# Optimization experiments

Hardware: AMD Instinct MI355X
Metric: run time of the kernel (lower is better)

The kernel has to match this reference:

```python
import jax, jax.numpy as jnp
import numpy as np
from jax import lax

L, B, F = 1024, 2, 1024
E = 2
H = E * F          # ssm_features = 2048
N = 16             # state_dim
R = F // N         # dt_rank = 64
K = 4              # conv kernel size
DT_MIN, DT_MAX = 0.001, 0.1


def setup_inputs() -> dict:
    key = jax.random.key(0)
    ks = jax.random.split(key, 6)
    def w(k, shape, fan_in):
        return jax.random.normal(k, shape, jnp.float32) / np.float32(np.sqrt(fan_in))
    x = jax.random.normal(ks[0], (L, B, F), jnp.float32)
    W_in = w(ks[1], (F, 2 * H), F)
    W_conv = w(ks[2], (K, H // E, H), K * (H // E))  # flax Conv kernel (K, in/groups, out), groups=E
    b_conv = jnp.zeros((H,), jnp.float32)
    A_log = jnp.log(jnp.broadcast_to(jnp.arange(1, N + 1, dtype=jnp.float32), (H, N)))
    D = jnp.ones((H,), jnp.float32)
    W_ssm = w(ks[3], (H, R + 2 * N), H)
    W_dt = w(ks[4], (R, H), R)
    b_dt = jnp.zeros((H,), jnp.float32)
    W_out = w(ks[5], (H, F), H)
    return dict(x=x, W_in=W_in, W_conv=W_conv, b_conv=b_conv, A_log=A_log, D=D,
                W_ssm=W_ssm, W_dt=W_dt, b_dt=b_dt, W_out=W_out)


def _selective_scan(u, dt, A, Bm, Cm, D):
    # u, dt: (L,B,H); A: (H,N); Bm, Cm: (L,B,N); D: (H,)
    dt = jnp.clip(dt, DT_MIN, DT_MAX)
    dA = jnp.exp(jnp.einsum('lbh,hn->lbhn', dt, A))          # (L,B,H,N)
    dBu = jnp.einsum('lbh,lbn->lbhn', dt * u, Bm)            # (L,B,H,N)
    def comb(s, c):
        return (c[0] * s[0], c[0] * s[1] + c[1])
    _, xs = lax.associative_scan(comb, (dA, dBu), axis=0)
    y = jnp.einsum('lbn,lbhn->lbh', Cm, xs)
    return y + u * D


def reference(x, W_in, W_conv, b_conv, A_log, D, W_ssm, W_dt, b_dt, W_out):
    # in_proj (no bias) then split into ssm branch and gate residual
    h = x @ W_in                                             # (L,B,2H)
    xs, res = jnp.split(h, 2, axis=-1)                       # each (L,B,H)
    # causal grouped conv over time: rearrange (L,B,H)->(B,L,H), NWC layout
    xc = jnp.transpose(xs, (1, 0, 2))
    xc = lax.conv_general_dilated(
        xc, W_conv, window_strides=(1,), padding=[(K - 1, 0)],
        dimension_numbers=('NWC', 'WIO', 'NWC'), feature_group_count=E) + b_conv
    xs = jnp.transpose(xc, (1, 0, 2))                        # (L,B,H)
    u = jax.nn.silu(xs)
    # SSM
    A = -jnp.exp(A_log)                                      # (H,N)
    proj = u @ W_ssm                                         # (L,B,N+N+R)
    Bm = proj[..., :N]
    Cm = proj[..., N:2 * N]
    dt = proj[..., 2 * N:]
    delta = jax.nn.softplus(dt @ W_dt + b_dt)                # (L,B,H)
    y = _selective_scan(u, delta, A, Bm, Cm, D)
    # gate and out_proj (no bias)
    return (y * jax.nn.silu(res)) @ W_out                    # (L,B,F)
```

## Files before the change

### kernel.cpp

```cpp
#include <hip/hip_runtime.h>
#include <math.h>


typedef unsigned short u16;
typedef unsigned int u32;
typedef __attribute__((ext_vector_type(8))) short short8;
typedef __attribute__((ext_vector_type(4))) float floatx4;
typedef __attribute__((ext_vector_type(4))) u16 ushort4v;

__device__ __forceinline__ u16 f2bf(float f) {
    u32 u = __float_as_uint(f);
    return (u16)((u + 0x7fffu + ((u >> 16) & 1u)) >> 16);
}
__device__ __forceinline__ float bf2f(u16 v) {
    return __uint_as_float((u32)v << 16);
}

__device__ __forceinline__ float dpp_red16(float v) {
    v += __uint_as_float((u32)__builtin_amdgcn_update_dpp(
        0, (int)__float_as_uint(v), 0xB1, 0xF, 0xF, true));
    v += __uint_as_float((u32)__builtin_amdgcn_update_dpp(
        0, (int)__float_as_uint(v), 0x4E, 0xF, 0xF, true));
    v += __uint_as_float((u32)__builtin_amdgcn_update_dpp(
        0, (int)__float_as_uint(v), 0x141, 0xF, 0xF, true));
    v += __uint_as_float((u32)__builtin_amdgcn_update_dpp(
        0, (int)__float_as_uint(v), 0x128, 0xF, 0xF, true));
    return v;
}

__device__ __forceinline__ void gl_lds16(const u16* g, u16* l) {
    auto gp = reinterpret_cast<const __attribute__((address_space(1))) u32*>(
        reinterpret_cast<uintptr_t>(g));
    auto lp = reinterpret_cast<__attribute__((address_space(3))) u32*>(
        reinterpret_cast<uintptr_t>(l));
    __builtin_amdgcn_global_load_lds(gp, lp, 16, 0, 0);
}

__global__ __launch_bounds__(256) void trans_k(const float* __restrict__ S,
                                               u16* __restrict__ D, int R, int C)
{
    __shared__ u16 t[64][65];
    int br = blockIdx.x * 64;
    int bc = blockIdx.y * 64;
    int c = threadIdx.x & 63;
    int r0 = threadIdx.x >> 6;
#pragma unroll
    for (int i = 0; i < 16; ++i) {
        int r = r0 + i * 4;
        float v = 0.f;
        if (br + r < R && bc + c < C) v = S[(size_t)(br + r) * C + bc + c];
        t[r][c] = f2bf(v);
    }
    __syncthreads();
    int cc0 = threadIdx.x >> 4;
    int rr0 = (threadIdx.x & 15) * 4;
#pragma unroll
    for (int i = 0; i < 4; ++i) {
        int cc = i * 16 + cc0;
        if (bc + cc < C) {
            ushort4v o;
#pragma unroll
            for (int k = 0; k < 4; ++k) o[k] = t[rr0 + k][cc];
            *(ushort4v*)(D + (size_t)(bc + cc) * R + br + rr0) = o;
        }
    }
}

__global__ __launch_bounds__(256) void tbf_k(const u16* __restrict__ S,
                                             u16* __restrict__ D)
{
    __shared__ u16 t[64][68];
    int br = blockIdx.x * 64;
    int bc = blockIdx.y * 64;
    int c = threadIdx.x & 63;
    int r0 = threadIdx.x >> 6;
#pragma unroll
    for (int i = 0; i < 16; ++i) {
        int r = r0 + i * 4;
        t[r][c] = S[(size_t)(br + r) * 2048 + bc + c];
    }
    __syncthreads();
#pragma unroll
    for (int i = 0; i < 16; ++i) {
        int r = r0 + i * 4;
        D[(size_t)(bc + r) * 2048 + br + c] = t[c][r];
    }
}

__global__ __launch_bounds__(256) void cvt_k(const float* __restrict__ S, u16* __restrict__ D)
{
    int i = (blockIdx.x * 256 + threadIdx.x) * 4;
    float4 v = *(const float4*)(S + i);
    u16 o[4] = {f2bf(v.x), f2bf(v.y), f2bf(v.z), f2bf(v.w)};
    *(ulong1*)(D + i) = *(ulong1*)o;
}

__global__ __launch_bounds__(256) void cvtp_k(const float* __restrict__ proj,
                                              u16* __restrict__ pb,
                                              u16* __restrict__ bc)
{
    if (blockIdx.x < 128) {
        int g = blockIdx.x * 256 + threadIdx.x;
        int m = g >> 4, i = (g & 15) * 4;
        float4 v = *(const float4*)(proj + (size_t)m * 128 + 64 + i);
        u16 o[4] = {f2bf(v.x), f2bf(v.y), f2bf(v.z), f2bf(v.w)};
        *(ulong1*)(pb + (size_t)m * 64 + i) = *(ulong1*)o;
    } else {
        int g = (blockIdx.x - 128) * 256 + threadIdx.x;
        int m = g >> 3, i = (g & 7) * 4;
        float4 v = *(const float4*)(proj + (size_t)m * 128 + i);
        u16 o[4] = {f2bf(v.x), f2bf(v.y), f2bf(v.z), f2bf(v.w)};
        *(ulong1*)(bc + (size_t)m * 32 + i) = *(ulong1*)o;
    }
}

template<int MODE>
__global__ __launch_bounds__(256) void gls_k(
    const u16* __restrict__ A, int lda,
    const u16* __restrict__ B, int ldb,
    float* __restrict__ Cf, int ldc,
    u16* __restrict__ Cb0, u16* __restrict__ Cb1,
    const float* __restrict__ bias, int nkt)
{
    __shared__ u16 As[128 * 64];
    __shared__ u16 Bs[64 * 64];
    const int tid = threadIdx.x;
    const int bm = blockIdx.y * 128;
    const int bn = blockIdx.x * 64;
    const int gofs = (MODE == 1 && bn >= 1024) ? 1024 : 0;
    const int lane = tid & 63, wave = tid >> 6, wm = wave * 32;
    const int m16 = lane & 15, q = lane >> 4;
    floatx4 acc[2][4] = {};

    const int rsub = lane >> 3;
    const int pch  = lane & 7;

    for (int kt = 0; kt < nkt; ++kt) {
        const int k0 = kt * 64;
        int tap = 0, ck = k0;
        if (MODE == 1) { tap = k0 >> 10; ck = k0 & 1023; }
#pragma unroll
        for (int i = 0; i < 4; ++i) {
            int r = i * 32 + wave * 8 + rsub;
            int c = pch ^ (r & 7);
            const u16* g;
            if (MODE == 1) {
                int rg = bm + r + 2 * tap - 6;
                g = A + (size_t)rg * lda + gofs + ck + c * 8;
            } else {
                g = A + (size_t)(bm + r) * lda + k0 + c * 8;
            }
            gl_lds16(g, As + i * 2048 + wave * 512);
        }
#pragma unroll
        for (int i = 0; i < 2; ++i) {
            int r = i * 32 + wave * 8 + rsub;
            int c = pch ^ (r & 7);
            gl_lds16(B + (size_t)(bn + r) * ldb + k0 + c * 8,
                     Bs + i * 2048 + wave * 512);
        }
        if (MODE == 1 && bm == 0) {
            int zr = 6 - 2 * tap;
            if (zr > 0) {
                asm volatile("s_waitcnt vmcnt(0)" ::: "memory");
                if (tid < 64) {
                    int r = tid >> 3;
                    if (r < zr) *(short8*)(As + r * 64 + (tid & 7) * 8) = short8{};
                }
            }
        }
        __syncthreads();

#pragma unroll
        for (int ks = 0; ks < 2; ++ks) {
            short8 af[2], bfr[4];
#pragma unroll
            for (int ti = 0; ti < 2; ++ti) {
                int r = wm + ti * 16 + m16;
                int p = (ks * 4 + q) ^ (r & 7);
                af[ti] = *(const short8*)(As + r * 64 + p * 8);
            }
#pragma unroll
            for (int tj = 0; tj < 4; ++tj) {
                int r = tj * 16 + m16;
                int p = (ks * 4 + q) ^ (r & 7);
                bfr[tj] = *(const short8*)(Bs + r * 64 + p * 8);
            }
#pragma unroll
            for (int ti = 0; ti < 2; ++ti)
#pragma unroll
                for (int tj = 0; tj < 4; ++tj)
                    acc[ti][tj] = __builtin_amdgcn_mfma_f32_16x16x32_bf16(
                        af[ti], bfr[tj], acc[ti][tj], 0, 0, 0);
        }
        __syncthreads();
    }

    if (MODE == 2) {
#pragma unroll
        for (int tj = 0; tj < 4; ++tj) {
            int gn = bn + tj * 16 + m16;
#pragma unroll
            for (int ti = 0; ti < 2; ++ti) {
                int gm0 = bm + wm + ti * 16 + q * 4;
#pragma unroll
                for (int r = 0; r < 4; ++r)
                    Cf[(size_t)(gm0 + r) * ldc + gn] = acc[ti][tj][r];
            }
        }
        return;
    }
    if (MODE == 0 && bn >= 2048) {
#pragma unroll
        for (int tj = 0; tj < 4; ++tj) {
            int gn = bn + tj * 16 + m16;
#pragma unroll
            for (int ti = 0; ti < 2; ++ti) {
                int gm0 = bm + wm + ti * 16 + q * 4;
                ushort4v h;
#pragma unroll
                for (int r = 0; r < 4; ++r) h[r] = f2bf(acc[ti][tj][r]);
                *(ushort4v*)(Cb1 + (size_t)(gn - 2048) * 2048 + gm0) = h;
            }
        }
        return;
    }
#pragma unroll
    for (int tj = 0; tj < 4; ++tj) {
        int gn = bn + tj * 16 + m16;
        float bv = (MODE == 1) ? bias[gn] : 0.f;
#pragma unroll
        for (int ti = 0; ti < 2; ++ti) {
            int lr0 = wm + ti * 16 + q * 4;
            ushort4v h;
#pragma unroll
            for (int r = 0; r < 4; ++r) {
                float v = acc[ti][tj][r];
                if (MODE == 1) {
                    v += bv;
                    v = v / (1.f + __expf(-v));
                }
                u16 hv = f2bf(v);
                h[r] = hv;
                As[(lr0 + r) * 64 + tj * 16 + m16] = hv;
            }
            if (MODE == 1)
                *(ushort4v*)(Cb1 + (size_t)gn * 2048 + bm + lr0) = h;
        }
    }
    __syncthreads();
    {
        int row = tid >> 1, half = tid & 1;
        u16* gdst = Cb0 + (size_t)(bm + row) * 2048 + bn + half * 32;
        const u16* lsrc = As + row * 64 + half * 32;
#pragma unroll
        for (int i = 0; i < 4; ++i)
            *(short8*)(gdst + i * 8) = *(const short8*)(lsrc + i * 8);
    }
}

#define APAD 40
__global__ __launch_bounds__(256) void g3_k(
    const u16* __restrict__ A,
    const u16* __restrict__ Bw,
    float* __restrict__ proj)
{
    __shared__ u16 As[128 * APAD];
    __shared__ u16 Bs[64 * APAD];
    const int tid = threadIdx.x;
    const int bn = blockIdx.x * 64;
    const int bm = blockIdx.y * 128;
    const int kb = blockIdx.z * 512;
    const int lane = tid & 63, wave = tid >> 6, wm = wave * 32;
    const int m16 = lane & 15, q = lane >> 4;
    floatx4 acc[2][4] = {};
    const int ar = tid >> 2, ac = (tid & 3) * 8;

    for (int kt = 0; kt < 16; ++kt) {
        const int k0 = kb + kt * 32;
#pragma unroll
        for (int p = 0; p < 2; ++p) {
            int r = ar + p * 64;
            *(short8*)(As + r * APAD + ac) =
                *(const short8*)(A + (size_t)(bm + r) * 2048 + k0 + ac);
        }
        *(short8*)(Bs + ar * APAD + ac) =
            *(const short8*)(Bw + (size_t)(bn + ar) * 2048 + k0 + ac);
        __syncthreads();

        short8 af[2], bfr[4];
#pragma unroll
        for (int ti = 0; ti < 2; ++ti)
            af[ti] = *(const short8*)(As + (wm + ti * 16 + m16) * APAD + q * 8);
#pragma unroll
        for (int tj = 0; tj < 4; ++tj)
            bfr[tj] = *(const short8*)(Bs + (tj * 16 + m16) * APAD + q * 8);
#pragma unroll
        for (int ti = 0; ti < 2; ++ti)
#pragma unroll
            for (int tj = 0; tj < 4; ++tj)
                acc[ti][tj] = __builtin_amdgcn_mfma_f32_16x16x32_bf16(
                    af[ti], bfr[tj], acc[ti][tj], 0, 0, 0);
        __syncthreads();
    }

#pragma unroll
    for (int tj = 0; tj < 4; ++tj) {
        int gn = bn + tj * 16 + m16;
        if (gn >= 96) continue;
        int col = (gn < 16) ? (2 * gn) : (gn < 32 ? 2 * (gn - 16) + 1 : 32 + gn);
#pragma unroll
        for (int ti = 0; ti < 2; ++ti)
#pragma unroll
            for (int r = 0; r < 4; ++r) {
                int gm = bm + wm + ti * 16 + q * 4 + r;
                atomicAdd(proj + (size_t)gm * 128 + col, acc[ti][tj][r]);
            }
    }
}

__global__ __launch_bounds__(256) void g4_k(
    const u16* __restrict__ A,
    const u16* __restrict__ B,
    const float* __restrict__ bias,
    float* __restrict__ Cf)
{
    __shared__ u16 As[128 * APAD];
    __shared__ u16 Bs[64 * APAD];
    const int tid = threadIdx.x;
    const int bm = blockIdx.y * 128;
    const int bn = blockIdx.x * 64;
    const int lane = tid & 63, wave = tid >> 6, wm = wave * 32;
    const int m16 = lane & 15, q = lane >> 4;
    floatx4 acc[2][4] = {};
    const int ar = tid >> 2, ac = (tid & 3) * 8;

    for (int kt = 0; kt < 2; ++kt) {
        const int k0 = kt * 32;
#pragma unroll
        for (int p = 0; p < 2; ++p) {
            int r = ar + p * 64;
            *(short8*)(As + r * APAD + ac) =
                *(const short8*)(A + (size_t)(bm + r) * 64 + k0 + ac);
        }
        *(short8*)(Bs + ar * APAD + ac) =
            *(const short8*)(B + (size_t)(bn + ar) * 64 + k0 + ac);
        __syncthreads();
        short8 af[2], bfr[4];
#pragma unroll
        for (int ti = 0; ti < 2; ++ti)
            af[ti] = *(const short8*)(As + (wm + ti * 16 + m16) * APAD + q * 8);
#pragma unroll
        for (int tj = 0; tj < 4; ++tj)
            bfr[tj] = *(const short8*)(Bs + (tj * 16 + m16) * APAD + q * 8);
#pragma unroll
        for (int ti = 0; ti < 2; ++ti)
#pragma unroll
            for (int tj = 0; tj < 4; ++tj)
                acc[ti][tj] = __builtin_amdgcn_mfma_f32_16x16x32_bf16(
                    af[ti], bfr[tj], acc[ti][tj], 0, 0, 0);
        __syncthreads();
    }
#pragma unroll
    for (int tj = 0; tj < 4; ++tj) {
        int gn = bn + tj * 16 + m16;
        float bv = bias[gn];
#pragma unroll
        for (int ti = 0; ti < 2; ++ti) {
            int gm0 = bm + wm + ti * 16 + q * 4;
            float t[4];
#pragma unroll
            for (int r = 0; r < 4; ++r) {
                float v = acc[ti][tj][r] + bv;
                v = (v > 15.f) ? v : log1pf(__expf(v));
                t[r] = fminf(fmaxf(v, 0.001f), 0.1f);
            }
            *(float4*)(Cf + (size_t)gn * 2048 + gm0) =
                make_float4(t[0], t[1], t[2], t[3]);
        }
    }
}

__global__ __launch_bounds__(512) void scan7_k(
    const float* __restrict__ deltaT,
    const u16* __restrict__ uT,
    const u16* __restrict__ bc16,
    const float* __restrict__ A_log,
    const float* __restrict__ Dvec,
    const u16* __restrict__ resT,
    u16* __restrict__ zT)
{
    __shared__ float lP[2][32][16], lS[2][32][16], lI[2][32][16];
    __shared__ float yrow[2048];
    const int h = blockIdx.x;
    const int tid = threadIdx.x;
    const int n = tid & 15;
    const int c = tid >> 4;
    const int l0 = c * 32;

    const float Ahn = -__expf(A_log[h * 16 + n]);
    const float* drow = deltaT + (size_t)h * 2048;
    const u16*   urow = uT     + (size_t)h * 2048;

    float s0 = 0.f, s1 = 0.f, T0 = 0.f, T1 = 0.f;
    for (int j = 0; j < 32; ++j) {
        int l = l0 + j;
        float2 dtv = *(const float2*)(drow + 2 * l);
        u32 uv = *(const u32*)(urow + 2 * l);
        float uu0 = __uint_as_float(uv << 16);
        float uu1 = __uint_as_float(uv & 0xffff0000u);
        u32 w0 = *(const u32*)(bc16 + (size_t)(2 * l) * 32 + 2 * n);
        u32 w1 = *(const u32*)(bc16 + (size_t)(2 * l + 1) * 32 + 2 * n);
        float e0 = __expf(dtv.x * Ahn);
        float e1 = __expf(dtv.y * Ahn);
        s0 = fmaf(e0, s0, dtv.x * uu0 * __uint_as_float(w0 << 16));
        s1 = fmaf(e1, s1, dtv.y * uu1 * __uint_as_float(w1 << 16));
        T0 += dtv.x;
        T1 += dtv.y;
    }
    lP[0][c][n] = __expf(T0 * Ahn); lS[0][c][n] = s0;
    lP[1][c][n] = __expf(T1 * Ahn); lS[1][c][n] = s1;
    __syncthreads();
    if (tid < 32) {
        int bb = tid >> 4, nn = tid & 15;
        float X = 0.f;
#pragma unroll
        for (int cc = 0; cc < 32; ++cc) {
            lI[bb][cc][nn] = X;
            X = fmaf(lP[bb][cc][nn], X, lS[bb][cc][nn]);
        }
    }
    __syncthreads();

    s0 = lI[0][c][n];
    s1 = lI[1][c][n];
    const float Dh = Dvec[h];
    for (int j = 0; j < 32; ++j) {
        int l = l0 + j;
        float2 dtv = *(const float2*)(drow + 2 * l);
        u32 uv = *(const u32*)(urow + 2 * l);
        float uu0 = __uint_as_float(uv << 16);
        float uu1 = __uint_as_float(uv & 0xffff0000u);
        u32 w0 = *(const u32*)(bc16 + (size_t)(2 * l) * 32 + 2 * n);
        u32 w1 = *(const u32*)(bc16 + (size_t)(2 * l + 1) * 32 + 2 * n);
        float e0 = __expf(dtv.x * Ahn);
        float e1 = __expf(dtv.y * Ahn);
        s0 = fmaf(e0, s0, dtv.x * uu0 * __uint_as_float(w0 << 16));
        s1 = fmaf(e1, s1, dtv.y * uu1 * __uint_as_float(w1 << 16));
        float v0 = dpp_red16(__uint_as_float(w0 & 0xffff0000u) * s0);
        float v1 = dpp_red16(__uint_as_float(w1 & 0xffff0000u) * s1);
        if (n == 0) {
            yrow[2 * l]     = v0 + uu0 * Dh;
            yrow[2 * l + 1] = v1 + uu1 * Dh;
        }
    }
    __syncthreads();
    {
        int t0 = tid * 4;
        ushort4v rv = *(const ushort4v*)(resT + (size_t)h * 2048 + t0);
        u16 o[4];
#pragma unroll
        for (int i = 0; i < 4; ++i) {
            float r = bf2f(rv[i]);
            float y = yrow[t0 + i];
            o[i] = f2bf(y * (r / (1.f + __expf(-r))));
        }
        *(ulong1*)(zT + (size_t)h * 2048 + t0) = *(ulong1*)o;
    }
}

extern "C" void kernel_launch(void* const* d_in, const int* in_sizes, int n_in,
                              void* d_out, int out_size, void* d_ws, size_t ws_size,
                              hipStream_t stream)
{
    const float* x      = (const float*)d_in[0];
    const float* W_in   = (const float*)d_in[1];
    const float* W_conv = (const float*)d_in[2];
    const float* b_conv = (const float*)d_in[3];
    const float* A_log  = (const float*)d_in[4];
    const float* Dv     = (const float*)d_in[5];
    const float* W_ssm  = (const float*)d_in[6];
    const float* W_dt   = (const float*)d_in[7];
    const float* b_dt   = (const float*)d_in[8];
    const float* W_out  = (const float*)d_in[9];
    float* out = (float*)d_out;

    char* wsc = (char*)d_ws;
    u16*   xb     = (u16*)wsc;
    float* projb  = (float*)wsc;
    u16*   pb_dt  = (u16*)(wsc + (2u << 20));
    u16*   bc16   = (u16*)(wsc + (3u << 20));
    u16*   WT_in  = (u16*)(wsc + (4u << 20));
    u16*   u_mh   = (u16*)(wsc + (4u << 20));
    u16*   z_mh   = (u16*)(wsc + (4u << 20));
    u16*   xsbf   = (u16*)(wsc + (12u << 20));
    u16*   zT     = xsbf;
    u16*   resT   = (u16*)(wsc + (20u << 20));
    u16*   WT_cv  = (u16*)(wsc + (28u << 20));
    float* deltaT = (float*)(wsc + (28u << 20));
    u16*   uT     = (u16*)(wsc + (44u << 20));
    u16*   WT_out = (u16*)(wsc + (52u << 20));
    u16*   WT_ssm = (u16*)(wsc + (56u << 20));
    u16*   WT_dt  = (u16*)(wsc + (56u << 20) + (512u << 10));

    dim3 blk(256);

    trans_k<<<dim3(64, 32), blk, 0, stream>>>(W_conv, WT_cv, 4096, 2048);
    trans_k<<<dim3(16, 64), blk, 0, stream>>>(W_in, WT_in, 1024, 4096);
    trans_k<<<dim3(32, 16), blk, 0, stream>>>(W_out, WT_out, 2048, 1024);
    trans_k<<<dim3(32, 2),  blk, 0, stream>>>(W_ssm, WT_ssm, 2048, 96);
    trans_k<<<dim3(1, 32),  blk, 0, stream>>>(W_dt, WT_dt, 64, 2048);
    cvt_k<<<dim3(2048), blk, 0, stream>>>(x, xb);

    gls_k<0><<<dim3(64, 16), blk, 0, stream>>>(
        xb, 1024, WT_in, 1024, nullptr, 0, xsbf, resT, nullptr, 16);

    gls_k<1><<<dim3(32, 16), blk, 0, stream>>>(
        xsbf, 2048, WT_cv, 4096, nullptr, 0, u_mh, uT, b_conv, 64);

    hipMemsetAsync(projb, 0, 2048 * 128 * sizeof(float), stream);
    g3_k<<<dim3(2, 16, 4), blk, 0, stream>>>(u_mh, WT_ssm, projb);

    cvtp_k<<<dim3(192), blk, 0, stream>>>(projb, pb_dt, bc16);

    g4_k<<<dim3(32, 16), blk, 0, stream>>>(pb_dt, WT_dt, b_dt, deltaT);

    scan7_k<<<dim3(2048), dim3(512), 0, stream>>>(
        deltaT, uT, bc16, A_log, Dv, resT, zT);

    tbf_k<<<dim3(32, 32), blk, 0, stream>>>(zT, z_mh);

    gls_k<2><<<dim3(16, 16), blk, 0, stream>>>(
        z_mh, 2048, WT_out, 2048, out, 1024, nullptr, nullptr, nullptr, 32);
}
```

Baseline: 359.7 us.

## Fuse prep kernels, split-K out projection and SSM GEMM, use exp2 in scan

```diff
diff --git a/kernel.cpp b/kernel.cpp
--- a/kernel.cpp
+++ b/kernel.cpp
@@ -36,12 +36,13 @@
     __builtin_amdgcn_global_load_lds(gp, lp, 16, 0, 0);
 }
 
-__global__ __launch_bounds__(256) void trans_k(const float* __restrict__ S,
-                                               u16* __restrict__ D, int R, int C)
+__device__ __forceinline__ void trans_dev(const float* __restrict__ S,
+                                          u16* __restrict__ D, int R, int C,
+                                          int bx, int by)
 {
     __shared__ u16 t[64][65];
-    int br = blockIdx.x * 64;
-    int bc = blockIdx.y * 64;
+    int br = bx * 64;
+    int bc = by * 64;
     int c = threadIdx.x & 63;
     int r0 = threadIdx.x >> 6;
 #pragma unroll
@@ -66,6 +67,33 @@
     }
 }
 
+__global__ __launch_bounds__(256) void prep_k(
+    const float* __restrict__ Wc, u16* __restrict__ WTc,
+    const float* __restrict__ Wi, u16* __restrict__ WTi,
+    const float* __restrict__ Wo, u16* __restrict__ WTo,
+    const float* __restrict__ Ws, u16* __restrict__ WTs,
+    const float* __restrict__ Wd, u16* __restrict__ WTd,
+    const float* __restrict__ x,  u16* __restrict__ xb)
+{
+    int b = blockIdx.x;
+    if (b < 2048) { trans_dev(Wc, WTc, 4096, 2048, b & 63, b >> 6); return; }
+    b -= 2048;
+    if (b < 1024) { trans_dev(Wi, WTi, 1024, 4096, b & 15, b >> 4); return; }
+    b -= 1024;
+    if (b < 512)  { trans_dev(Wo, WTo, 2048, 1024, b & 31, b >> 5); return; }
+    b -= 512;
+    if (b < 64)   { trans_dev(Ws, WTs, 2048, 96,   b & 31, b >> 5); return; }
+    b -= 64;
+    if (b < 32)   { trans_dev(Wd, WTd, 64, 2048,   0,      b);      return; }
+    b -= 32;
+    {
+        int i = (b * 256 + threadIdx.x) * 4;
+        float4 v = *(const float4*)(x + i);
+        u16 o[4] = {f2bf(v.x), f2bf(v.y), f2bf(v.z), f2bf(v.w)};
+        *(ulong1*)(xb + i) = *(ulong1*)o;
+    }
+}
+
 __global__ __launch_bounds__(256) void tbf_k(const u16* __restrict__ S,
                                              u16* __restrict__ D)
 {
@@ -85,14 +113,6 @@
         int r = r0 + i * 4;
         D[(size_t)(bc + r) * 2048 + br + c] = t[c][r];
     }
-}
-
-__global__ __launch_bounds__(256) void cvt_k(const float* __restrict__ S, u16* __restrict__ D)
-{
-    int i = (blockIdx.x * 256 + threadIdx.x) * 4;
-    float4 v = *(const float4*)(S + i);
-    u16 o[4] = {f2bf(v.x), f2bf(v.y), f2bf(v.z), f2bf(v.w)};
-    *(ulong1*)(D + i) = *(ulong1*)o;
 }
 
 __global__ __launch_bounds__(256) void cvtp_k(const float* __restrict__ proj,
@@ -127,6 +147,7 @@
     const int tid = threadIdx.x;
     const int bm = blockIdx.y * 128;
     const int bn = blockIdx.x * 64;
+    const int kofs = (MODE == 3) ? blockIdx.z * nkt * 64 : 0;
     const int gofs = (MODE == 1 && bn >= 1024) ? 1024 : 0;
     const int lane = tid & 63, wave = tid >> 6, wm = wave * 32;
     const int m16 = lane & 15, q = lane >> 4;
@@ -136,7 +157,7 @@
     const int pch  = lane & 7;
 
     for (int kt = 0; kt < nkt; ++kt) {
-        const int k0 = kt * 64;
+        const int k0 = kofs + kt * 64;
         int tap = 0, ck = k0;
         if (MODE == 1) { tap = k0 >> 10; ck = k0 & 1023; }
 #pragma unroll
@@ -196,7 +217,7 @@
         __syncthreads();
     }
 
-    if (MODE == 2) {
+    if (MODE == 3) {
 #pragma unroll
         for (int tj = 0; tj < 4; ++tj) {
             int gn = bn + tj * 16 + m16;
@@ -205,7 +226,7 @@
                 int gm0 = bm + wm + ti * 16 + q * 4;
 #pragma unroll
                 for (int r = 0; r < 4; ++r)
-                    Cf[(size_t)(gm0 + r) * ldc + gn] = acc[ti][tj][r];
+                    atomicAdd(Cf + (size_t)(gm0 + r) * ldc + gn, acc[ti][tj][r]);
             }
         }
         return;
@@ -270,13 +291,13 @@
     const int tid = threadIdx.x;
     const int bn = blockIdx.x * 64;
     const int bm = blockIdx.y * 128;
-    const int kb = blockIdx.z * 512;
+    const int kb = blockIdx.z * 256;
     const int lane = tid & 63, wave = tid >> 6, wm = wave * 32;
     const int m16 = lane & 15, q = lane >> 4;
     floatx4 acc[2][4] = {};
     const int ar = tid >> 2, ac = (tid & 3) * 8;
 
-    for (int kt = 0; kt < 16; ++kt) {
+    for (int kt = 0; kt < 8; ++kt) {
         const int k0 = kb + kt * 32;
 #pragma unroll
         for (int p = 0; p < 2; ++p) {
@@ -398,7 +419,7 @@
     const int c = tid >> 4;
     const int l0 = c * 32;
 
-    const float Ahn = -__expf(A_log[h * 16 + n]);
+    const float An2 = -__expf(A_log[h * 16 + n]) * 1.442695041f;
     const float* drow = deltaT + (size_t)h * 2048;
     const u16*   urow = uT     + (size_t)h * 2048;
 
@@ -411,15 +432,15 @@
         float uu1 = __uint_as_float(uv & 0xffff0000u);
         u32 w0 = *(const u32*)(bc16 + (size_t)(2 * l) * 32 + 2 * n);
         u32 w1 = *(const u32*)(bc16 + (size_t)(2 * l + 1) * 32 + 2 * n);
-        float e0 = __expf(dtv.x * Ahn);
-        float e1 = __expf(dtv.y * Ahn);
+        float e0 = exp2f(dtv.x * An2);
+        float e1 = exp2f(dtv.y * An2);
         s0 = fmaf(e0, s0, dtv.x * uu0 * __uint_as_float(w0 << 16));
         s1 = fmaf(e1, s1, dtv.y * uu1 * __uint_as_float(w1 << 16));
         T0 += dtv.x;
         T1 += dtv.y;
     }
-    lP[0][c][n] = __expf(T0 * Ahn); lS[0][c][n] = s0;
-    lP[1][c][n] = __expf(T1 * Ahn); lS[1][c][n] = s1;
+    lP[0][c][n] = exp2f(T0 * An2); lS[0][c][n] = s0;
+    lP[1][c][n] = exp2f(T1 * An2); lS[1][c][n] = s1;
     __syncthreads();
     if (tid < 32) {
         int bb = tid >> 4, nn = tid & 15;
@@ -443,8 +464,8 @@
         float uu1 = __uint_as_float(uv & 0xffff0000u);
         u32 w0 = *(const u32*)(bc16 + (size_t)(2 * l) * 32 + 2 * n);
         u32 w1 = *(const u32*)(bc16 + (size_t)(2 * l + 1) * 32 + 2 * n);
-        float e0 = __expf(dtv.x * Ahn);
-        float e1 = __expf(dtv.y * Ahn);
+        float e0 = exp2f(dtv.x * An2);
+        float e1 = exp2f(dtv.y * An2);
         s0 = fmaf(e0, s0, dtv.x * uu0 * __uint_as_float(w0 << 16));
         s1 = fmaf(e1, s1, dtv.y * uu1 * __uint_as_float(w1 << 16));
         float v0 = dpp_red16(__uint_as_float(w0 & 0xffff0000u) * s0);
@@ -505,21 +526,21 @@
 
     dim3 blk(256);
 
-    trans_k<<<dim3(64, 32), blk, 0, stream>>>(W_conv, WT_cv, 4096, 2048);
-    trans_k<<<dim3(16, 64), blk, 0, stream>>>(W_in, WT_in, 1024, 4096);
-    trans_k<<<dim3(32, 16), blk, 0, stream>>>(W_out, WT_out, 2048, 1024);
-    trans_k<<<dim3(32, 2),  blk, 0, stream>>>(W_ssm, WT_ssm, 2048, 96);
-    trans_k<<<dim3(1, 32),  blk, 0, stream>>>(W_dt, WT_dt, 64, 2048);
-    cvt_k<<<dim3(2048), blk, 0, stream>>>(x, xb);
+    prep_k<<<dim3(5728), blk, 0, stream>>>(
+        W_conv, WT_cv, W_in, WT_in, W_out, WT_out, W_ssm, WT_ssm, W_dt, WT_dt,
+        x, xb);
+
+    hipMemsetAsync(out, 0, 2048 * 1024 * sizeof(float), stream);
 
     gls_k<0><<<dim3(64, 16), blk, 0, stream>>>(
         xb, 1024, WT_in, 1024, nullptr, 0, xsbf, resT, nullptr, 16);
 
+    hipMemsetAsync(projb, 0, 2048 * 128 * sizeof(float), stream);
+
     gls_k<1><<<dim3(32, 16), blk, 0, stream>>>(
         xsbf, 2048, WT_cv, 4096, nullptr, 0, u_mh, uT, b_conv, 64);
 
-    hipMemsetAsync(projb, 0, 2048 * 128 * sizeof(float), stream);
-    g3_k<<<dim3(2, 16, 4), blk, 0, stream>>>(u_mh, WT_ssm, projb);
+    g3_k<<<dim3(2, 16, 8), blk, 0, stream>>>(u_mh, WT_ssm, projb);
 
     cvtp_k<<<dim3(192), blk, 0, stream>>>(projb, pb_dt, bc16);
 
@@ -530,6 +551,6 @@
 
     tbf_k<<<dim3(32, 32), blk, 0, stream>>>(zT, z_mh);
 
-    gls_k<2><<<dim3(16, 16), blk, 0, stream>>>(
-        z_mh, 2048, WT_out, 2048, out, 1024, nullptr, nullptr, nullptr, 32);
-}
+    gls_k<3><<<dim3(16, 16, 2), blk, 0, stream>>>(
+        z_mh, 2048, WT_out, 2048, out, 1024, nullptr, nullptr, nullptr, 16);
+}
```

Measured after the change: 339.5 us. -5.6%, faster.
